# Optimization experiments

Measured on AMD Instinct MI355X. Metric: run time of the kernel, lower is better.

## Reference

```python
import jax, jax.numpy as jnp
import numpy as np

K = 512          # num_embeddings
D = 64           # embedding_dim
BETA = 0.25      # commitment_cost
DECAY = 0.99
EPS = 1e-5


def setup_inputs() -> dict:
    key = jax.random.key(0)
    k1, k2, k3 = jax.random.split(key, 3)
    inputs = jax.random.normal(k1, (64, D, 32, 32), dtype=jnp.float32)  # NCHW, C == embedding_dim
    embedding = jax.random.normal(k2, (K, D), dtype=jnp.float32)
    ema_w = jax.random.normal(k3, (K, D), dtype=jnp.float32)
    ema_cluster_size = jnp.zeros((K,), dtype=jnp.float32)
    return {"inputs": inputs, "embedding": embedding, "ema_w": ema_w,
            "ema_cluster_size": ema_cluster_size}


def reference(inputs, embedding, ema_w, ema_cluster_size):
    # NCHW -> NHWC, flatten to [N, D]
    x = jnp.transpose(inputs, (0, 2, 3, 1))
    B, H, W, C = x.shape
    flat = x.reshape(-1, C)                                   # [N, D]

    # squared L2 distances to all codes: [N, K]
    d = (jnp.sum(flat * flat, axis=1, keepdims=True)
         + jnp.sum(embedding * embedding, axis=1)
         - 2.0 * flat @ embedding.T)
    idx = jnp.argmin(d, axis=1)                               # [N]

    # gather (equivalent to one-hot @ embedding, without materializing one-hot)
    quantized = embedding[idx].reshape(x.shape)               # [B,H,W,D]

    # EMA codebook update (training branch); segment sums replace encodings.T matmuls
    counts = jax.ops.segment_sum(jnp.ones_like(idx, dtype=flat.dtype), idx,
                                 num_segments=K)              # [K]
    new_cs = ema_cluster_size * DECAY + (1.0 - DECAY) * counts
    n = jnp.sum(new_cs)
    new_cs = (new_cs + EPS) / (n + K * EPS) * n               # Laplace smoothing
    dw = jax.ops.segment_sum(flat, idx, num_segments=K)       # [K, D]
    new_ema_w = ema_w * DECAY + (1.0 - DECAY) * dw
    new_embedding = new_ema_w / new_cs[:, None]

    # commitment loss + straight-through estimator
    e_latent_loss = jnp.mean((jax.lax.stop_gradient(quantized) - x) ** 2)
    loss = BETA * e_latent_loss
    quantized_st = x + jax.lax.stop_gradient(quantized - x)

    avg_probs = counts / flat.shape[0]
    perplexity = jnp.exp(-jnp.sum(avg_probs * jnp.log(avg_probs + 1e-10)))

    out_q = jnp.transpose(quantized_st, (0, 3, 1, 2))         # back to NCHW
    return (loss, out_q, perplexity, idx.reshape(B, H, W),
            new_cs, new_ema_w, new_embedding)
```

## Files before the change

### kernel.cpp

```cpp
#include <hip/hip_runtime.h>

#define K_CODES 512
#define DIM 64
#define HW 1024
#define NVEC 65536

#define O0 0
#define O1 1
#define O2 4194305
#define O3 4194306
#define O4 4259842
#define O5 4260354
#define O6 4293122

#define WS_EE  64
#define WS_CNT 1024
#define WS_DW  2048
#define WS_BP  35840
#define XSS    72

typedef __bf16 bf16x8 __attribute__((ext_vector_type(8)));
typedef float  f32x4  __attribute__((ext_vector_type(4)));

__global__ void k0_init(const float* __restrict__ emb, float* __restrict__ wsf) {
    const int b = blockIdx.x, t = threadIdx.x;
    if (b < 128) {
        wsf[WS_DW + b * 256 + t] = 0.0f;
    } else if (b == 128) {
        int* cnt = (int*)(wsf + WS_CNT);
        cnt[t] = 0; cnt[t + 256] = 0;
        if (t == 0) wsf[0] = 0.0f;
    } else if (b < 131) {
        int k = (b - 129) * 256 + t;
        const float* e = emb + k * DIM;
        float s = 0.0f;
        #pragma unroll
        for (int c = 0; c < DIM; ++c) s += e[c] * e[c];
        wsf[WS_EE + k] = s;
    } else {
        int g = (b - 131) * 256 + t;
        int j    = g & 7;
        int lane = (g >> 3) & 63;
        int ks   = (g >> 9) & 1;
        int rest = g >> 10;
        int ntg  = rest & 31;
        int s    = rest >> 5;
        int code = ntg * 16 + (lane & 15);
        int c    = ks * 32 + (lane >> 4) * 8 + j;
        float v = -2.0f * emb[code * DIM + c];
        __bf16 h0 = (__bf16)v;  float r1 = v  - (float)h0;
        __bf16 h1 = (__bf16)r1; float r2 = r1 - (float)h1;
        __bf16 hv = (s == 0) ? h0 : (s == 1 ? h1 : (__bf16)r2);
        ((__bf16*)(wsf + WS_BP))[g] = hv;
    }
}

__global__ __launch_bounds__(512, 2)
void k1_main(const float* __restrict__ in, const float* __restrict__ emb,
             float* __restrict__ out, float* __restrict__ wsf) {
    __shared__ float xs[128 * XSS];
    __shared__ float pmin[4][128];
    __shared__ int   pidx[4][128];
    __shared__ float xxs[128];
    __shared__ int   hist[K_CODES];

    const int t    = threadIdx.x;
    const int lane = t & 63;
    const int wave = t >> 6;
    const int mi2  = wave & 1;
    const int ni2  = wave >> 1;
    const int col  = lane & 15;
    const int quad = lane >> 4;

    hist[t] = 0;

    const int blk     = blockIdx.x;
    const int n_img   = blk >> 3;
    const int hw_base = (blk & 7) * 128;
    const float* xbase = in + n_img * (DIM * HW) + hw_base;

    #pragma unroll
    for (int rep = 0; rep < 16; ++rep) {
        int e = rep * 512 + t;
        int c = e >> 7, h0 = e & 127;
        xs[h0 * XSS + c] = xbase[c * HW + h0];
    }

    f32x4 acc[4][8];
    #pragma unroll
    for (int nt = 0; nt < 8; ++nt) {
        float eev = wsf[WS_EE + ni2 * 128 + nt * 16 + col];
        #pragma unroll
        for (int mi = 0; mi < 4; ++mi) {
            acc[mi][nt][0] = eev; acc[mi][nt][1] = eev;
            acc[mi][nt][2] = eev; acc[mi][nt][3] = eev;
        }
    }

    __syncthreads();

    if (t < 128) {
        float s = 0.0f;
        #pragma unroll
        for (int c = 0; c < DIM; ++c) { float v = xs[t * XSS + c]; s += v * v; }
        xxs[t] = s;
    }

    const bf16x8* bp8 = (const bf16x8*)(wsf + WS_BP);

    #pragma unroll
    for (int ks = 0; ks < 2; ++ks) {
        bf16x8 A0[4], A1[4], A2[4];
        #pragma unroll
        for (int mi = 0; mi < 4; ++mi) {
            const float* src = &xs[(mi2 * 64 + mi * 16 + col) * XSS + ks * 32 + quad * 8];
            #pragma unroll
            for (int j = 0; j < 8; ++j) {
                float v = src[j];
                __bf16 h0 = (__bf16)v;  float r1 = v  - (float)h0;
                __bf16 h1 = (__bf16)r1; float r2 = r1 - (float)h1;
                A0[mi][j] = h0; A1[mi][j] = h1; A2[mi][j] = (__bf16)r2;
            }
        }
        #pragma unroll
        for (int s = 0; s < 3; ++s) {
            bf16x8 Bv[8];
            #pragma unroll
            for (int nt = 0; nt < 8; ++nt)
                Bv[nt] = bp8[(((s * 32 + ni2 * 8 + nt) * 2 + ks) * 64) + lane];
            #pragma unroll
            for (int mi = 0; mi < 4; ++mi)
                #pragma unroll
                for (int nt = 0; nt < 8; ++nt)
                    acc[mi][nt] = __builtin_amdgcn_mfma_f32_16x16x32_bf16(A0[mi], Bv[nt], acc[mi][nt], 0, 0, 0);
            if (s < 2) {
                #pragma unroll
                for (int mi = 0; mi < 4; ++mi)
                    #pragma unroll
                    for (int nt = 0; nt < 8; ++nt)
                        acc[mi][nt] = __builtin_amdgcn_mfma_f32_16x16x32_bf16(A1[mi], Bv[nt], acc[mi][nt], 0, 0, 0);
            }
            if (s == 0) {
                #pragma unroll
                for (int mi = 0; mi < 4; ++mi)
                    #pragma unroll
                    for (int nt = 0; nt < 8; ++nt)
                        acc[mi][nt] = __builtin_amdgcn_mfma_f32_16x16x32_bf16(A2[mi], Bv[nt], acc[mi][nt], 0, 0, 0);
            }
        }
    }

    #pragma unroll
    for (int mi = 0; mi < 4; ++mi) {
        #pragma unroll
        for (int r = 0; r < 4; ++r) {
            float v  = acc[mi][0][r];
            int   bi = ni2 * 128 + col;
            #pragma unroll
            for (int nt = 1; nt < 8; ++nt) {
                float u  = acc[mi][nt][r];
                int   ui = ni2 * 128 + nt * 16 + col;
                if (u < v) { v = u; bi = ui; }
            }
            #pragma unroll
            for (int off = 1; off < 16; off <<= 1) {
                float ov = __shfl_xor(v, off);
                int   oi = __shfl_xor(bi, off);
                if (ov < v || (ov == v && oi < bi)) { v = ov; bi = oi; }
            }
            if (col == 0) {
                int row = mi2 * 64 + mi * 16 + quad * 4 + r;
                pmin[ni2][row] = v;
                pidx[ni2][row] = bi;
            }
        }
    }
    __syncthreads();

    if (t < 128) {
        float v = pmin[0][t]; int bi = pidx[0][t];
        #pragma unroll
        for (int q = 1; q < 4; ++q) {
            float u = pmin[q][t]; int ui = pidx[q][t];
            if (u < v) { v = u; bi = ui; }
        }
        pidx[0][t] = bi;
        out[O3 + blk * 128 + t] = (float)bi;
        atomicAdd(&hist[bi], 1);
        float ld = v + xxs[t];
        #pragma unroll
        for (int off = 32; off > 0; off >>= 1) ld += __shfl_down(ld, off);
        if ((t & 63) == 0) atomicAdd(wsf + 0, ld);
    }
    __syncthreads();

    {
        int v = t & 127, cq = t >> 7;
        int kv = pidx[0][v];
        const float* ew = emb + kv * DIM;
        float* oq = out + O1 + n_img * (DIM * HW) + hw_base + v;
        #pragma unroll
        for (int c = cq * 16; c < cq * 16 + 16; ++c) oq[c * HW] = ew[c];
    }

    {
        float* dw = wsf + WS_DW;
        #pragma unroll 1
        for (int v = wave * 16; v < wave * 16 + 16; ++v) {
            int kv = pidx[0][v];
            atomicAdd(&dw[kv * DIM + lane], xs[v * XSS + lane]);
        }
    }

    int* cnt = (int*)(wsf + WS_CNT);
    if (hist[t]) atomicAdd(&cnt[t], hist[t]);
}

__global__ void k2a(const float* __restrict__ ema_cs, float* __restrict__ out,
                    const float* __restrict__ wsf) {
    __shared__ float s1[512], s2[512];
    const int t = threadIdx.x;
    const int* cnt = (const int*)(wsf + WS_CNT);
    float c   = (float)cnt[t];
    float raw = 0.99f * ema_cs[t] + 0.01f * c;
    float p   = c * (1.0f / 65536.0f);
    s1[t] = raw;
    s2[t] = p * logf(p + 1e-10f);
    __syncthreads();
    for (int s = 256; s > 0; s >>= 1) {
        if (t < s) { s1[t] += s1[t + s]; s2[t] += s2[t + s]; }
        __syncthreads();
    }
    float n = s1[0];
    float smooth = (raw + 1e-5f) / (n + 512.0f * 1e-5f) * n;
    out[O4 + t] = smooth;
    if (t == 0) {
        out[O2] = expf(-s2[0]);
        out[O0] = 0.25f * wsf[0] * (1.0f / 4194304.0f);
    }
}

__global__ void k2b(const float* __restrict__ ema_w, const float* __restrict__ wsf,
                    float* __restrict__ out) {
    const int m = blockIdx.x * 256 + threadIdx.x;
    const int k = m >> 6;
    float w = 0.99f * ema_w[m] + 0.01f * wsf[WS_DW + m];
    out[O5 + m] = w;
    out[O6 + m] = w / out[O4 + k];
}

extern "C" void kernel_launch(void* const* d_in, const int* in_sizes, int n_in,
                              void* d_out, int out_size, void* d_ws, size_t ws_size,
                              hipStream_t stream) {
    const float* in     = (const float*)d_in[0];
    const float* emb    = (const float*)d_in[1];
    const float* ema_w  = (const float*)d_in[2];
    const float* ema_cs = (const float*)d_in[3];
    float* out = (float*)d_out;
    float* wsf = (float*)d_ws;

    hipLaunchKernelGGL(k0_init, dim3(515), dim3(256), 0, stream, emb, wsf);
    hipLaunchKernelGGL(k1_main, dim3(512), dim3(512), 0, stream, in, emb, out, wsf);
    hipLaunchKernelGGL(k2a,     dim3(1),   dim3(512), 0, stream, ema_cs, out, wsf);
    hipLaunchKernelGGL(k2b,     dim3(128), dim3(256), 0, stream, ema_w, wsf, out);
}
```

Measured before the change: 162.4 us.

## Replace atomic segment sums with per-code ballot scan kernel and separate gather

The main kernel stops doing global float atomics for the codebook sums, LDS histogram atomics and global loss atomics. Instead it writes the indices and per-block loss partials to workspace, and stages the transposed NHWC input into the quantized output buffer as scratch. A new per-code kernel scans all 65536 indices with wave ballots to accumulate counts and feature sums deterministically. A separate gather kernel then overwrites the output with codebook rows. The trade is removing atomic contention in exchange for each of 512 blocks reading the full index array (256 KB) plus extra launches and an extra write and read of the 16 MB activation.

```diff
diff --git a/kernel.cpp b/kernel.cpp
--- a/kernel.cpp
+++ b/kernel.cpp
@@ -13,32 +13,29 @@
 #define O5 4260354
 #define O6 4293122
 
-#define WS_EE  64
-#define WS_CNT 1024
-#define WS_DW  2048
-#define WS_BP  35840
-#define XSS    72
+#define WS_LOSS 0
+#define WS_CNT  512
+#define WS_EE   1024
+#define WS_IDX  1536
+#define WS_DW   67072
+#define WS_BP   99840
+#define XSS     65
 
 typedef __bf16 bf16x8 __attribute__((ext_vector_type(8)));
 typedef float  f32x4  __attribute__((ext_vector_type(4)));
+typedef float  f32x4v __attribute__((ext_vector_type(4)));
 
 __global__ void k0_init(const float* __restrict__ emb, float* __restrict__ wsf) {
     const int b = blockIdx.x, t = threadIdx.x;
-    if (b < 128) {
-        wsf[WS_DW + b * 256 + t] = 0.0f;
-    } else if (b == 128) {
-        int* cnt = (int*)(wsf + WS_CNT);
-        cnt[t] = 0; cnt[t + 256] = 0;
-        if (t == 0) wsf[0] = 0.0f;
-    } else if (b < 131) {
-        int k = (b - 129) * 256 + t;
+    if (b < 2) {
+        int k = b * 256 + t;
         const float* e = emb + k * DIM;
         float s = 0.0f;
         #pragma unroll
         for (int c = 0; c < DIM; ++c) s += e[c] * e[c];
         wsf[WS_EE + k] = s;
     } else {
-        int g = (b - 131) * 256 + t;
+        int g = (b - 2) * 256 + t;
         int j    = g & 7;
         int lane = (g >> 3) & 63;
         int ks   = (g >> 9) & 1;
@@ -62,7 +59,7 @@
     __shared__ float pmin[4][128];
     __shared__ int   pidx[4][128];
     __shared__ float xxs[128];
-    __shared__ int   hist[K_CODES];
+    __shared__ float lossp[2];
 
     const int t    = threadIdx.x;
     const int lane = t & 63;
@@ -71,8 +68,6 @@
     const int ni2  = wave >> 1;
     const int col  = lane & 15;
     const int quad = lane >> 4;
-
-    hist[t] = 0;
 
     const int blk     = blockIdx.x;
     const int n_img   = blk >> 3;
@@ -184,51 +179,93 @@
             float u = pmin[q][t]; int ui = pidx[q][t];
             if (u < v) { v = u; bi = ui; }
         }
-        pidx[0][t] = bi;
         out[O3 + blk * 128 + t] = (float)bi;
-        atomicAdd(&hist[bi], 1);
+        ((int*)(wsf + WS_IDX))[blk * 128 + t] = bi;
         float ld = v + xxs[t];
         #pragma unroll
         for (int off = 32; off > 0; off >>= 1) ld += __shfl_down(ld, off);
-        if ((t & 63) == 0) atomicAdd(wsf + 0, ld);
-    }
-    __syncthreads();
-
-    {
-        int v = t & 127, cq = t >> 7;
-        int kv = pidx[0][v];
-        const float* ew = emb + kv * DIM;
-        float* oq = out + O1 + n_img * (DIM * HW) + hw_base + v;
-        #pragma unroll
-        for (int c = cq * 16; c < cq * 16 + 16; ++c) oq[c * HW] = ew[c];
-    }
-
-    {
-        float* dw = wsf + WS_DW;
-        #pragma unroll 1
-        for (int v = wave * 16; v < wave * 16 + 16; ++v) {
-            int kv = pidx[0][v];
-            atomicAdd(&dw[kv * DIM + lane], xs[v * XSS + lane]);
-        }
-    }
-
-    int* cnt = (int*)(wsf + WS_CNT);
-    if (hist[t]) atomicAdd(&cnt[t], hist[t]);
+        if ((t & 63) == 0) lossp[t >> 6] = ld;
+    }
+    __syncthreads();
+    if (t == 0) wsf[WS_LOSS + blk] = lossp[0] + lossp[1];
+
+    float* xq = out + O1 + blk * (128 * 64);
+    #pragma unroll
+    for (int rep = 0; rep < 16; ++rep) {
+        int g = rep * 512 + t;
+        int row = g >> 6, c = g & 63;
+        xq[g] = xs[row * XSS + c];
+    }
+}
+
+__global__ __launch_bounds__(256, 4)
+void k_dw(const float* __restrict__ xq, const int* __restrict__ idxw,
+          float* __restrict__ wsf) {
+    __shared__ float sacc[4][64];
+    __shared__ int   scnt[4];
+    const int t = threadIdx.x, lane = t & 63, w = t >> 6;
+    const int code = blockIdx.x;
+
+    float acc = 0.0f;
+    int   cnt = 0;
+    const int* ip = idxw + w * 16384;
+    #pragma unroll 4
+    for (int r = 0; r < 256; ++r) {
+        int iv = ip[r * 64 + lane];
+        unsigned long long m = __ballot(iv == code);
+        cnt += (int)__popcll(m);
+        while (m) {
+            int s = __ffsll((long long)m) - 1; m &= m - 1;
+            int vid = w * 16384 + r * 64 + s;
+            acc += xq[vid * 64 + lane];
+        }
+    }
+    sacc[w][lane] = acc;
+    if (lane == 0) scnt[w] = cnt;
+    __syncthreads();
+    if (w == 0) {
+        float a = sacc[0][lane] + sacc[1][lane] + sacc[2][lane] + sacc[3][lane];
+        wsf[WS_DW + code * 64 + lane] = a;
+        if (lane == 0)
+            wsf[WS_CNT + code] = (float)(scnt[0] + scnt[1] + scnt[2] + scnt[3]);
+    }
+}
+
+__global__ __launch_bounds__(256, 4)
+void k_q(const float* __restrict__ emb, const int* __restrict__ idxw,
+         float* __restrict__ out) {
+    const int t    = threadIdx.x;
+    const int lane = t & 63;
+    const int cg   = t >> 6;
+    const int b    = blockIdx.x;
+    const int n    = b >> 4;
+    const int hw0  = (b & 15) * 64;
+
+    int iv = idxw[n * HW + hw0 + lane];
+    const f32x4v* er = (const f32x4v*)(emb + iv * DIM + cg * 16);
+    f32x4v e0 = er[0], e1 = er[1], e2 = er[2], e3 = er[3];
+    float ev[16];
+    #pragma unroll
+    for (int j = 0; j < 4; ++j) { ev[j] = e0[j]; ev[4+j] = e1[j]; ev[8+j] = e2[j]; ev[12+j] = e3[j]; }
+
+    float* ob = out + O1 + n * (DIM * HW) + hw0 + lane;
+    #pragma unroll
+    for (int j = 0; j < 16; ++j) ob[(cg * 16 + j) * HW] = ev[j];
 }
 
 __global__ void k2a(const float* __restrict__ ema_cs, float* __restrict__ out,
                     const float* __restrict__ wsf) {
-    __shared__ float s1[512], s2[512];
+    __shared__ float s1[512], s2[512], s3[512];
     const int t = threadIdx.x;
-    const int* cnt = (const int*)(wsf + WS_CNT);
-    float c   = (float)cnt[t];
+    float c   = wsf[WS_CNT + t];
     float raw = 0.99f * ema_cs[t] + 0.01f * c;
     float p   = c * (1.0f / 65536.0f);
     s1[t] = raw;
     s2[t] = p * logf(p + 1e-10f);
+    s3[t] = wsf[WS_LOSS + t];
     __syncthreads();
     for (int s = 256; s > 0; s >>= 1) {
-        if (t < s) { s1[t] += s1[t + s]; s2[t] += s2[t + s]; }
+        if (t < s) { s1[t] += s1[t + s]; s2[t] += s2[t + s]; s3[t] += s3[t + s]; }
         __syncthreads();
     }
     float n = s1[0];
@@ -236,7 +273,7 @@
     out[O4 + t] = smooth;
     if (t == 0) {
         out[O2] = expf(-s2[0]);
-        out[O0] = 0.25f * wsf[0] * (1.0f / 4194304.0f);
+        out[O0] = 0.25f * s3[0] * (1.0f / 4194304.0f);
     }
 }
 
@@ -258,9 +295,12 @@
     const float* ema_cs = (const float*)d_in[3];
     float* out = (float*)d_out;
     float* wsf = (float*)d_ws;
-
-    hipLaunchKernelGGL(k0_init, dim3(515), dim3(256), 0, stream, emb, wsf);
-    hipLaunchKernelGGL(k1_main, dim3(512), dim3(512), 0, stream, in, emb, out, wsf);
-    hipLaunchKernelGGL(k2a,     dim3(1),   dim3(512), 0, stream, ema_cs, out, wsf);
-    hipLaunchKernelGGL(k2b,     dim3(128), dim3(256), 0, stream, ema_w, wsf, out);
-}
+    const int* idxw = (const int*)(wsf + WS_IDX);
+
+    hipLaunchKernelGGL(k0_init, dim3(386),  dim3(256), 0, stream, emb, wsf);
+    hipLaunchKernelGGL(k1_main, dim3(512),  dim3(512), 0, stream, in, emb, out, wsf);
+    hipLaunchKernelGGL(k_dw,    dim3(512),  dim3(256), 0, stream, out + O1, idxw, wsf);
+    hipLaunchKernelGGL(k_q,     dim3(1024), dim3(256), 0, stream, emb, idxw, out);
+    hipLaunchKernelGGL(k2a,     dim3(1),    dim3(512), 0, stream, ema_cs, out, wsf);
+    hipLaunchKernelGGL(k2b,     dim3(128),  dim3(256), 0, stream, ema_w, wsf, out);
+}
```

After: 307.5 us. 89.4% more time.
